# Performance work log

Measured on AMD Instinct MI355X. Metric: run time of the kernel, lower is better.

## Reference

```python
import jax, jax.numpy as jnp
import numpy as np

EPS = 0.1        # SinkhornDistance eps (hard-coded in SGE.__init__)
MAX_ITER = 10    # SinkhornDistance max_iter
THRESH = 0.1     # early-exit threshold in SinkhornDistance.forward
N_POINTS = 32
SPACE_DIM = 16   # emb_dim // n_points = 512 // 32


def _sinkhorn_cost(x, y):
    """Regularized OT cost between point clouds x, y: [B, P, D] -> [B]."""
    # C[b,i,j] = sum_d |x[b,i,d] - y[b,j,d]|^2
    C = jnp.sum(jnp.square(jnp.abs(x[:, :, None, :] - y[:, None, :, :])), axis=-1)
    B, P1 = x.shape[0], x.shape[1]
    P2 = y.shape[1]
    mu = jnp.full((B, P1), 1.0 / P1, dtype=x.dtype)
    nu = jnp.full((B, P2), 1.0 / P2, dtype=x.dtype)

    def M(u, v):
        # (-C + u_i + v_j) / eps
        return (-C + u[:, :, None] + v[:, None, :]) / EPS

    def step(carry, _):
        u, v, done = carry
        u_new = EPS * (jnp.log(mu + 1e-8) - jax.nn.logsumexp(M(u, v), axis=-1)) + u
        v_new = EPS * (jnp.log(nu + 1e-8)
                       - jax.nn.logsumexp(M(u_new, v).swapaxes(-2, -1), axis=-1)) + v
        err = jnp.mean(jnp.sum(jnp.abs(u_new - u), axis=-1))
        u2 = jnp.where(done, u, u_new)
        v2 = jnp.where(done, v, v_new)
        done2 = done | (err < THRESH)  # torch breaks AFTER applying the update
        return (u2, v2, done2), None

    init = (jnp.zeros_like(mu), jnp.zeros_like(nu), jnp.array(False))
    (u, v, _), _ = jax.lax.scan(step, init, None, length=MAX_ITER)
    pi = jnp.exp(M(u, v))
    return jnp.sum(pi * C, axis=(-2, -1))  # [B]


def setup_inputs() -> dict:
    key = jax.random.key(0)
    k1, k2, k3, k4 = jax.random.split(key, 4)
    n_nodes, feat, emb, n_edges = 10000, 256, 512, 4096
    x = jax.random.normal(k1, (n_nodes, feat), dtype=jnp.float32)
    W = jax.random.normal(k2, (feat, emb), dtype=jnp.float32) / np.float32(np.sqrt(feat))
    edges_pos = jax.random.randint(k3, (2, n_edges), 0, n_nodes)
    edges_neg = jax.random.randint(k4, (2, n_edges), 0, n_nodes)
    return {"x": x, "W": W, "edges_pos": edges_pos, "edges_neg": edges_neg}


def reference(x, W, edges_pos, edges_neg):
    z = x @ W  # encoder: linear projection [n_nodes, emb_dim]

    def score_pairs(nx, ny):
        a = z[nx].reshape(-1, N_POINTS, SPACE_DIM)
        b = z[ny].reshape(-1, N_POINTS, SPACE_DIM)
        return -_sinkhorn_cost(a, b)

    pos_energy = score_pairs(edges_pos[0], edges_pos[1])
    neg_energy = score_pairs(edges_neg[0], edges_neg[1])
    loss = jnp.mean(pos_energy ** 2 + jnp.exp(neg_energy))
    return loss
```

## Files before the change

kernel.cpp:

```cpp
#include <hip/hip_runtime.h>
#include <hip/hip_bf16.h>
#include <math.h>

#define N_POINTS 32
#define SPACE_DIM 16
#define EMB 512
#define THRESH 0.1f
#define MAX_ITER 10

#define NEG10LOG2E -14.42695040888963f
#define EPS_LN2     0.0693147180559945f
#define LOGMU2     -4.99999953834f

typedef _Float16 half8 __attribute__((ext_vector_type(8)));
typedef float floatx4 __attribute__((ext_vector_type(4)));

__global__ __launch_bounds__(256) void convert_f16(
    const float* __restrict__ X, const float* __restrict__ W,
    _Float16* __restrict__ Xh, _Float16* __restrict__ WhT,
    int MK, int K, int N, int total)
{
    int idx = blockIdx.x * 256 + threadIdx.x;
    if (idx < MK) {
        Xh[idx] = (_Float16)X[idx];
    } else if (idx < total) {
        int f = idx - MK;
        int n = f / K;
        int k = f - n * K;
        WhT[f] = (_Float16)W[(size_t)k * N + n];
    }
}

__global__ __launch_bounds__(256) void gemm_mfma_f16(
    const _Float16* __restrict__ Xh, const _Float16* __restrict__ WhT,
    float* __restrict__ Z, int M, int K, int N)
{
    int t = threadIdx.x;
    int wave = t >> 6;
    int lane = t & 63;
    int quad = lane >> 4;
    int l16 = lane & 15;

    int mrow = blockIdx.x * 64 + wave * 16 + l16;
    int msafe = mrow < M ? mrow : M - 1;
    int n0 = blockIdx.y * 64;

    const _Float16* arow  = Xh + (size_t)msafe * K + quad * 8;
    const _Float16* bcol0 = WhT + (size_t)(n0 + l16) * K + quad * 8;

    floatx4 acc[4] = {{0.f,0.f,0.f,0.f},{0.f,0.f,0.f,0.f},
                      {0.f,0.f,0.f,0.f},{0.f,0.f,0.f,0.f}};

    for (int k0 = 0; k0 < K; k0 += 32) {
        half8 a = *(const half8*)(arow + k0);
        #pragma unroll
        for (int ct = 0; ct < 4; ++ct) {
            half8 b = *(const half8*)(bcol0 + (size_t)ct * 16 * K + k0);
            acc[ct] = __builtin_amdgcn_mfma_f32_16x16x32_f16(a, b, acc[ct], 0, 0, 0);
        }
    }

    int rbase = blockIdx.x * 64 + wave * 16 + quad * 4;
    #pragma unroll
    for (int ct = 0; ct < 4; ++ct) {
        int col = n0 + ct * 16 + l16;
        #pragma unroll
        for (int r = 0; r < 4; ++r) {
            int row = rbase + r;
            if (row < M) Z[(size_t)row * N + col] = acc[ct][r];
        }
    }
}

#define WPB 4

__global__ __launch_bounds__(256, 4) void sinkhorn_fused(
    const float* __restrict__ Z,
    const int* __restrict__ ep, const int* __restrict__ en,
    int nE,
    float* __restrict__ err_part,
    float* __restrict__ cost_all)
{
    __shared__ float shm[WPB][32 * 36];
    __shared__ float uvs[WPB][64];

    int tid = threadIdx.x;
    int wv = tid >> 6;
    int t = tid & 63;
    int b = blockIdx.x * WPB + wv;

    int side = (b >= nE) ? 1 : 0;
    int e = b - side * nE;
    const int* edges = side ? en : ep;
    int nx = edges[e];
    int ny = edges[e + nE];

    int c = t & 31;
    int h = t >> 5;
    int r0 = h * 16;

    float* sb  = shm[wv];
    float* csh = shm[wv];
    float* Ul  = uvs[wv];
    float* Vl  = uvs[wv] + 32;

    {
        const float4* zb4 = (const float4*)(Z + (size_t)ny * EMB);
        float4 q0 = zb4[t * 2];
        float4 q1 = zb4[t * 2 + 1];
        float* dst = sb + (t >> 1) * 20 + (t & 1) * 8;
        ((float4*)dst)[0] = q0;
        ((float4*)dst)[1] = q1;
    }
    float areg[16];
    {
        const float4* za4 = (const float4*)(Z + (size_t)nx * EMB + c * SPACE_DIM);
        float4 a0 = za4[0], a1 = za4[1], a2 = za4[2], a3 = za4[3];
        areg[0]=a0.x; areg[1]=a0.y; areg[2]=a0.z; areg[3]=a0.w;
        areg[4]=a1.x; areg[5]=a1.y; areg[6]=a1.z; areg[7]=a1.w;
        areg[8]=a2.x; areg[9]=a2.y; areg[10]=a2.z; areg[11]=a2.w;
        areg[12]=a3.x; areg[13]=a3.y; areg[14]=a3.z; areg[15]=a3.w;
    }

    float Crow[16];
    #pragma unroll
    for (int jj = 0; jj < 16; ++jj) {
        const float* bp = sb + (r0 + jj) * 20;
        float s = 0.f;
        #pragma unroll
        for (int d = 0; d < SPACE_DIM; ++d) {
            float diff = areg[d] - bp[d];
            s = fmaf(diff, diff, s);
        }
        Crow[jj] = s * NEG10LOG2E;
    }
    #pragma unroll
    for (int g = 0; g < 4; ++g) {
        *(float4*)&csh[c * 36 + r0 + g * 4] =
            make_float4(Crow[g*4+0], Crow[g*4+1], Crow[g*4+2], Crow[g*4+3]);
    }
    float Ccol[16];
    #pragma unroll
    for (int ii = 0; ii < 16; ++ii)
        Ccol[ii] = csh[(r0 + ii) * 36 + c];

    Vl[c] = 0.f;
    float U = 0.f;

    for (int it = 0; it < MAX_ITER; ++it) {
        float w[16];
        {
            const float4* vp = (const float4*)(Vl + r0);
            float4 v0 = vp[0], v1 = vp[1], v2 = vp[2], v3 = vp[3];
            float vv[16] = {v0.x,v0.y,v0.z,v0.w, v1.x,v1.y,v1.z,v1.w,
                            v2.x,v2.y,v2.z,v2.w, v3.x,v3.y,v3.z,v3.w};
            #pragma unroll
            for (int jj = 0; jj < 16; ++jj) w[jj] = Crow[jj] + vv[jj];
        }
        float mx = w[0];
        #pragma unroll
        for (int jj = 1; jj < 16; ++jj) mx = fmaxf(mx, w[jj]);
        mx = fmaxf(mx, __shfl_xor(mx, 32));
        float sm = 0.f, pc = 0.f;
        #pragma unroll
        for (int jj = 0; jj < 16; ++jj) {
            float ex = __builtin_amdgcn_exp2f(w[jj] - mx);
            sm += ex;
            pc = fmaf(ex, Crow[jj], pc);
        }
        sm += __shfl_xor(sm, 32);

        if (it > 0) {
            float cc = __builtin_amdgcn_exp2f(U + mx) * pc;
            #pragma unroll
            for (int m = 1; m < 64; m <<= 1) cc += __shfl_xor(cc, m);
            if (t == 0)
                cost_all[(size_t)(it - 1) * (2 * nE) + b] = -EPS_LN2 * cc;
        }

        float Un = LOGMU2 - (mx + __builtin_amdgcn_logf(sm));
        float du = fabsf(Un - U);
        #pragma unroll
        for (int m = 1; m < 32; m <<= 1) du += __shfl_xor(du, m);
        if (t == 0) err_part[(size_t)it * (2 * nE) + b] = EPS_LN2 * du;
        U = Un;
        Ul[c] = U;

        float wc[16];
        {
            const float4* up = (const float4*)(Ul + r0);
            float4 u0 = up[0], u1 = up[1], u2 = up[2], u3 = up[3];
            float uu[16] = {u0.x,u0.y,u0.z,u0.w, u1.x,u1.y,u1.z,u1.w,
                            u2.x,u2.y,u2.z,u2.w, u3.x,u3.y,u3.z,u3.w};
            #pragma unroll
            for (int ii = 0; ii < 16; ++ii) wc[ii] = Ccol[ii] + uu[ii];
        }
        float mx2 = wc[0];
        #pragma unroll
        for (int ii = 1; ii < 16; ++ii) mx2 = fmaxf(mx2, wc[ii]);
        mx2 = fmaxf(mx2, __shfl_xor(mx2, 32));
        float sm2 = 0.f;
        #pragma unroll
        for (int ii = 0; ii < 16; ++ii) sm2 += __builtin_amdgcn_exp2f(wc[ii] - mx2);
        sm2 += __shfl_xor(sm2, 32);
        float Vn = LOGMU2 - (mx2 + __builtin_amdgcn_logf(sm2));
        Vl[c] = Vn;
    }

    {
        const float4* vp = (const float4*)(Vl + r0);
        float4 v0 = vp[0], v1 = vp[1], v2 = vp[2], v3 = vp[3];
        float vv[16] = {v0.x,v0.y,v0.z,v0.w, v1.x,v1.y,v1.z,v1.w,
                        v2.x,v2.y,v2.z,v2.w, v3.x,v3.y,v3.z,v3.w};
        float cc = 0.f;
        #pragma unroll
        for (int jj = 0; jj < 16; ++jj)
            cc = fmaf(__builtin_amdgcn_exp2f(U + Crow[jj] + vv[jj]), Crow[jj], cc);
        #pragma unroll
        for (int m = 1; m < 64; m <<= 1) cc += __shfl_xor(cc, m);
        if (t == 0)
            cost_all[(size_t)(MAX_ITER - 1) * (2 * nE) + b] = -EPS_LN2 * cc;
    }
}

__global__ __launch_bounds__(256) void err_reduce(
    const float* __restrict__ err_part, float* __restrict__ err_mean, int nE)
{
    int side = blockIdx.x / MAX_ITER;
    int it = blockIdx.x - side * MAX_ITER;
    const float* p = err_part + (size_t)it * (2 * nE) + side * nE;
    float s = 0.f;
    for (int idx = threadIdx.x; idx < nE; idx += 256) s += p[idx];
    __shared__ float red[256];
    red[threadIdx.x] = s;
    __syncthreads();
    for (int stride = 128; stride > 0; stride >>= 1) {
        if (threadIdx.x < stride) red[threadIdx.x] += red[threadIdx.x + stride];
        __syncthreads();
    }
    if (threadIdx.x == 0) err_mean[side * MAX_ITER + it] = red[0] / (float)nE;
}

__global__ __launch_bounds__(256) void final_loss(
    const float* __restrict__ err_mean, const float* __restrict__ cost_all,
    float* __restrict__ out, int nE)
{
    int Tp = MAX_ITER, Tn = MAX_ITER;
    for (int it = 0; it < MAX_ITER; ++it)
        if (err_mean[it] < THRESH) { Tp = it + 1; break; }
    for (int it = 0; it < MAX_ITER; ++it)
        if (err_mean[MAX_ITER + it] < THRESH) { Tn = it + 1; break; }

    float s = 0.f;
    for (int b = threadIdx.x; b < 2 * nE; b += 256) {
        int side = (b >= nE) ? 1 : 0;
        int T = side ? Tn : Tp;
        float cost = cost_all[(size_t)(T - 1) * (2 * nE) + b];
        s += side ? expf(-cost) : cost * cost;
    }
    __shared__ float red[256];
    red[threadIdx.x] = s;
    __syncthreads();
    for (int stride = 128; stride > 0; stride >>= 1) {
        if (threadIdx.x < stride) red[threadIdx.x] += red[threadIdx.x + stride];
        __syncthreads();
    }
    if (threadIdx.x == 0) out[0] = red[0] / (float)nE;
}

extern "C" void kernel_launch(void* const* d_in, const int* in_sizes, int n_in,
                              void* d_out, int out_size, void* d_ws, size_t ws_size,
                              hipStream_t stream)
{
    const float* X = (const float*)d_in[0];
    const float* W = (const float*)d_in[1];
    const int* ep = (const int*)d_in[2];
    const int* en = (const int*)d_in[3];
    float* out = (float*)d_out;

    int K = in_sizes[1] / EMB;
    int M = in_sizes[0] / K;
    int nE = in_sizes[2] / 2;
    int MK = M * K;
    int total = MK + K * EMB;

    float* ws = (float*)d_ws;
    float* Z = ws;
    float* after_Z = Z + (size_t)M * EMB;
    _Float16* Xh = (_Float16*)after_Z;
    _Float16* WhT = Xh + (size_t)MK;
    float* err_part = (float*)(WhT + (size_t)K * EMB);
    float* cost_all = err_part + (size_t)MAX_ITER * 2 * nE;
    float* err_mean = cost_all + (size_t)MAX_ITER * 2 * nE;

    convert_f16<<<(total + 255) / 256, 256, 0, stream>>>(X, W, Xh, WhT, MK, K, EMB, total);

    dim3 gg((M + 63) / 64, EMB / 64);
    gemm_mfma_f16<<<gg, 256, 0, stream>>>(Xh, WhT, Z, M, K, EMB);

    int nblk = (2 * nE) / WPB;
    sinkhorn_fused<<<nblk, 64 * WPB, 0, stream>>>(Z, ep, en, nE, err_part, cost_all);
    err_reduce<<<2 * MAX_ITER, 256, 0, stream>>>(err_part, err_mean, nE);
    final_loss<<<1, 256, 0, stream>>>(err_mean, cost_all, out, nE);
}
```

Baseline: 159.7 us.

## Fuse fp16 conversion into GEMM and merge final reduction kernels

```diff
diff --git a/kernel.cpp b/kernel.cpp
--- a/kernel.cpp
+++ b/kernel.cpp
@@ -13,29 +13,44 @@
 #define LOGMU2     -4.99999953834f
 
 typedef _Float16 half8 __attribute__((ext_vector_type(8)));
+typedef _Float16 half4 __attribute__((ext_vector_type(4)));
 typedef float floatx4 __attribute__((ext_vector_type(4)));
 
-__global__ __launch_bounds__(256) void convert_f16(
+#define BSTRIDE 264
+
+__global__ __launch_bounds__(256) void gemm_fused(
     const float* __restrict__ X, const float* __restrict__ W,
-    _Float16* __restrict__ Xh, _Float16* __restrict__ WhT,
-    int MK, int K, int N, int total)
+    float* __restrict__ Z, int M, int K, int N, unsigned* __restrict__ counter)
 {
-    int idx = blockIdx.x * 256 + threadIdx.x;
-    if (idx < MK) {
-        Xh[idx] = (_Float16)X[idx];
-    } else if (idx < total) {
-        int f = idx - MK;
-        int n = f / K;
-        int k = f - n * K;
-        WhT[f] = (_Float16)W[(size_t)k * N + n];
-    }
-}
-
-__global__ __launch_bounds__(256) void gemm_mfma_f16(
-    const _Float16* __restrict__ Xh, const _Float16* __restrict__ WhT,
-    float* __restrict__ Z, int M, int K, int N)
-{
+    if (blockIdx.x == 0 && blockIdx.y == 0 && threadIdx.x == 0) counter[0] = 0u;
+
+    __shared__ _Float16 Bs[64][BSTRIDE];
+
     int t = threadIdx.x;
+    int n0 = blockIdx.y * 64;
+
+    #pragma unroll
+    for (int s = 0; s < 4; ++s) {
+        int u = s * 256 + t;
+        int nb = u & 15;
+        int kb = u >> 4;
+        float4 r0v = *(const float4*)&W[(size_t)(kb * 4 + 0) * N + n0 + nb * 4];
+        float4 r1v = *(const float4*)&W[(size_t)(kb * 4 + 1) * N + n0 + nb * 4];
+        float4 r2v = *(const float4*)&W[(size_t)(kb * 4 + 2) * N + n0 + nb * 4];
+        float4 r3v = *(const float4*)&W[(size_t)(kb * 4 + 3) * N + n0 + nb * 4];
+        float c0[4] = {r0v.x, r0v.y, r0v.z, r0v.w};
+        float c1[4] = {r1v.x, r1v.y, r1v.z, r1v.w};
+        float c2[4] = {r2v.x, r2v.y, r2v.z, r2v.w};
+        float c3[4] = {r3v.x, r3v.y, r3v.z, r3v.w};
+        #pragma unroll
+        for (int c = 0; c < 4; ++c) {
+            half4 h = {(_Float16)c0[c], (_Float16)c1[c],
+                       (_Float16)c2[c], (_Float16)c3[c]};
+            *(half4*)&Bs[nb * 4 + c][kb * 4] = h;
+        }
+    }
+    __syncthreads();
+
     int wave = t >> 6;
     int lane = t & 63;
     int quad = lane >> 4;
@@ -43,19 +58,19 @@
 
     int mrow = blockIdx.x * 64 + wave * 16 + l16;
     int msafe = mrow < M ? mrow : M - 1;
-    int n0 = blockIdx.y * 64;
-
-    const _Float16* arow  = Xh + (size_t)msafe * K + quad * 8;
-    const _Float16* bcol0 = WhT + (size_t)(n0 + l16) * K + quad * 8;
+    const float4* xp = (const float4*)(X + (size_t)msafe * K);
 
     floatx4 acc[4] = {{0.f,0.f,0.f,0.f},{0.f,0.f,0.f,0.f},
                       {0.f,0.f,0.f,0.f},{0.f,0.f,0.f,0.f}};
 
     for (int k0 = 0; k0 < K; k0 += 32) {
-        half8 a = *(const half8*)(arow + k0);
+        float4 lo = xp[(k0 >> 2) + quad * 2];
+        float4 hi = xp[(k0 >> 2) + quad * 2 + 1];
+        half8 a = {(_Float16)lo.x, (_Float16)lo.y, (_Float16)lo.z, (_Float16)lo.w,
+                   (_Float16)hi.x, (_Float16)hi.y, (_Float16)hi.z, (_Float16)hi.w};
         #pragma unroll
         for (int ct = 0; ct < 4; ++ct) {
-            half8 b = *(const half8*)(bcol0 + (size_t)ct * 16 * K + k0);
+            half8 b = *(const half8*)&Bs[ct * 16 + l16][k0 + quad * 8];
             acc[ct] = __builtin_amdgcn_mfma_f32_16x16x32_f16(a, b, acc[ct], 0, 0, 0);
         }
     }
@@ -223,43 +238,56 @@
     }
 }
 
-__global__ __launch_bounds__(256) void err_reduce(
-    const float* __restrict__ err_part, float* __restrict__ err_mean, int nE)
+__global__ __launch_bounds__(256) void err_final(
+    const float* __restrict__ err_part, const float* __restrict__ cost_all,
+    float* __restrict__ err_mean, unsigned* __restrict__ counter,
+    float* __restrict__ out, int nE)
 {
+    __shared__ float red[256];
+    __shared__ int is_last;
+
     int side = blockIdx.x / MAX_ITER;
     int it = blockIdx.x - side * MAX_ITER;
     const float* p = err_part + (size_t)it * (2 * nE) + side * nE;
     float s = 0.f;
     for (int idx = threadIdx.x; idx < nE; idx += 256) s += p[idx];
-    __shared__ float red[256];
     red[threadIdx.x] = s;
     __syncthreads();
     for (int stride = 128; stride > 0; stride >>= 1) {
         if (threadIdx.x < stride) red[threadIdx.x] += red[threadIdx.x + stride];
         __syncthreads();
     }
-    if (threadIdx.x == 0) err_mean[side * MAX_ITER + it] = red[0] / (float)nE;
-}
-
-__global__ __launch_bounds__(256) void final_loss(
-    const float* __restrict__ err_mean, const float* __restrict__ cost_all,
-    float* __restrict__ out, int nE)
-{
+    if (threadIdx.x == 0) {
+        __hip_atomic_store(&err_mean[side * MAX_ITER + it], red[0] / (float)nE,
+                           __ATOMIC_RELAXED, __HIP_MEMORY_SCOPE_AGENT);
+        __threadfence();
+        unsigned old = __hip_atomic_fetch_add(counter, 1u, __ATOMIC_ACQ_REL,
+                                              __HIP_MEMORY_SCOPE_AGENT);
+        is_last = (old == 2 * MAX_ITER - 1);
+    }
+    __syncthreads();
+    if (!is_last) return;
+
+    float em[2 * MAX_ITER];
+    #pragma unroll
+    for (int i = 0; i < 2 * MAX_ITER; ++i)
+        em[i] = __hip_atomic_load(&err_mean[i], __ATOMIC_RELAXED,
+                                  __HIP_MEMORY_SCOPE_AGENT);
     int Tp = MAX_ITER, Tn = MAX_ITER;
-    for (int it = 0; it < MAX_ITER; ++it)
-        if (err_mean[it] < THRESH) { Tp = it + 1; break; }
-    for (int it = 0; it < MAX_ITER; ++it)
-        if (err_mean[MAX_ITER + it] < THRESH) { Tn = it + 1; break; }
-
-    float s = 0.f;
+    for (int i = 0; i < MAX_ITER; ++i)
+        if (em[i] < THRESH) { Tp = i + 1; break; }
+    for (int i = 0; i < MAX_ITER; ++i)
+        if (em[MAX_ITER + i] < THRESH) { Tn = i + 1; break; }
+
+    float acc = 0.f;
     for (int b = threadIdx.x; b < 2 * nE; b += 256) {
-        int side = (b >= nE) ? 1 : 0;
-        int T = side ? Tn : Tp;
+        int sd = (b >= nE) ? 1 : 0;
+        int T = sd ? Tn : Tp;
         float cost = cost_all[(size_t)(T - 1) * (2 * nE) + b];
-        s += side ? expf(-cost) : cost * cost;
-    }
-    __shared__ float red[256];
-    red[threadIdx.x] = s;
+        acc += sd ? expf(-cost) : cost * cost;
+    }
+    __syncthreads();
+    red[threadIdx.x] = acc;
     __syncthreads();
     for (int stride = 128; stride > 0; stride >>= 1) {
         if (threadIdx.x < stride) red[threadIdx.x] += red[threadIdx.x + stride];
@@ -281,25 +309,20 @@
     int K = in_sizes[1] / EMB;
     int M = in_sizes[0] / K;
     int nE = in_sizes[2] / 2;
-    int MK = M * K;
-    int total = MK + K * EMB;
 
     float* ws = (float*)d_ws;
     float* Z = ws;
-    float* after_Z = Z + (size_t)M * EMB;
-    _Float16* Xh = (_Float16*)after_Z;
-    _Float16* WhT = Xh + (size_t)MK;
-    float* err_part = (float*)(WhT + (size_t)K * EMB);
+    float* err_part = Z + (size_t)M * EMB;
     float* cost_all = err_part + (size_t)MAX_ITER * 2 * nE;
     float* err_mean = cost_all + (size_t)MAX_ITER * 2 * nE;
-
-    convert_f16<<<(total + 255) / 256, 256, 0, stream>>>(X, W, Xh, WhT, MK, K, EMB, total);
+    unsigned* counter = (unsigned*)(err_mean + 32);
 
     dim3 gg((M + 63) / 64, EMB / 64);
-    gemm_mfma_f16<<<gg, 256, 0, stream>>>(Xh, WhT, Z, M, K, EMB);
+    gemm_fused<<<gg, 256, 0, stream>>>(X, W, Z, M, K, EMB, counter);
 
     int nblk = (2 * nE) / WPB;
     sinkhorn_fused<<<nblk, 64 * WPB, 0, stream>>>(Z, ep, en, nE, err_part, cost_all);
-    err_reduce<<<2 * MAX_ITER, 256, 0, stream>>>(err_part, err_mean, nE);
-    final_loss<<<1, 256, 0, stream>>>(err_mean, cost_all, out, nE);
+
+    err_final<<<2 * MAX_ITER, 256, 0, stream>>>(err_part, cost_all, err_mean,
+                                                counter, out, nE);
 }
```

Result: faster. 146.5 us (-8.3%).
